# Kernel tuning notes

Measured on AMD Instinct MI355X. Metric: run time of the kernel, lower is better.

The kernel has to match this reference:

```python
import jax, jax.numpy as jnp
import numpy as np

H_IMG, W_IMG = 48, 64  # feature-map resolution hard-coded in the module
NUM_HEADS = 8


def get_positional_encodings(B, N, dtype=jnp.float32):
    # (p3^2, p4^2, p3*p4, p3, p4, 1) on normalized grid; intrinsics=None path
    ys = jnp.linspace(-1.0, 1.0, H_IMG, dtype=dtype)
    xs = jnp.linspace(-1.0, 1.0, W_IMG, dtype=dtype)
    p3 = jnp.tile(ys, W_IMG)           # [N] = ys repeated W times (torch repeat)
    p4 = jnp.repeat(xs, H_IMG)         # [N] = each x repeated H times
    pos = jnp.stack([p3 * p3, p4 * p4, p3 * p4, p3, p4, jnp.ones_like(p3)], axis=-1)  # [N,6]
    return jnp.broadcast_to(pos[None], (B, N, 6))


def setup_inputs() -> dict:
    key = jax.random.key(0)
    k1, k2, k3, k4, k5 = jax.random.split(key, 5)
    B, N, C = 2, H_IMG * W_IMG, 256
    s = 0.02
    return {
        "x1": jax.random.normal(k1, (B, N, C), jnp.float32),
        "x2": jax.random.normal(k2, (B, N, C), jnp.float32),
        "Wq": jax.random.normal(k3, (C, C), jnp.float32) * s,      # qkv (one-way: q only)
        "Wkv": jax.random.normal(k4, (C, 2 * C), jnp.float32) * s,  # qkv2 -> k,v
        "Wpf": jax.random.normal(k5, (C + 6 * NUM_HEADS, C), jnp.float32) * s,  # proj_fundamental
        "bpf": jnp.zeros((C,), jnp.float32),
    }


def reference(x1, x2, Wq, Wkv, Wpf, bpf):
    B, N, C = x1.shape
    H = NUM_HEADS
    d = C // H
    scale = d ** -0.5

    # q from x1; k,v from x2 (separate linear, matching torch reshape/permute split)
    q1 = (x1 @ Wq).reshape(B, N, H, d).transpose(0, 2, 1, 3)          # [B,H,N,d]
    kv = (x2 @ Wkv).reshape(B, N, 2, H, d)
    k2 = kv[:, :, 0].transpose(0, 2, 1, 3)                            # [B,H,N,d]
    v2 = kv[:, :, 1].transpose(0, 2, 1, 3)                            # [B,H,N,d]

    attn = jax.nn.softmax(jnp.einsum('bhnd,bhmd->bhnm', q1, k2) * scale, axis=-1)  # [B,H,N,N]

    pos = get_positional_encodings(B, N, x1.dtype)                    # [B,N,6]
    v2p = jnp.concatenate(
        [v2, jnp.broadcast_to(pos[:, None], (B, H, N, 6))], axis=-1)  # [B,H,N,d+6]

    y = jnp.einsum('bhnm,bhmd->bhnd', attn, v2p)                      # [B,H,N,d+6]
    y = y.transpose(0, 2, 1, 3).reshape(B, N, H * (d + 6))            # [B,N,C+6H]
    y = y @ Wpf + bpf                                                 # [B,N,C]
    y = y.reshape(B, N, H, d).transpose(0, 2, 1, 3)                   # [B,H,N,d]

    return jnp.concatenate([attn, y], axis=-1)                        # [B,H,N,N+d]
```

## Files before the change

kernel.cpp:

```cpp
#include <hip/hip_runtime.h>
#include <hip/hip_bf16.h>
#include <cstdint>
#include <cstddef>

#define NB 2
#define NH 8
#define BHN 16
#define NN 3072
#define CC 256
#define DD 32
#define OUTW 3104
#define VW 48
#define KP 384

typedef __attribute__((ext_vector_type(8))) __bf16 bf16x8;
typedef __attribute__((ext_vector_type(4))) short short4v;
typedef __attribute__((ext_vector_type(4))) float f32x4;

static __device__ __forceinline__ unsigned short f2bf(float f) {
    __hip_bfloat16 h = __float2bfloat16(f);
    return *reinterpret_cast<unsigned short*>(&h);
}

static __device__ __forceinline__ bf16x8 ldb8(const unsigned short* p) {
    return *(const bf16x8*)p;
}

static __device__ __forceinline__ f32x4 mfma16(bf16x8 a, bf16x8 b, f32x4 c) {
    return __builtin_amdgcn_mfma_f32_16x16x32_bf16(a, b, c, 0, 0, 0);
}

__global__ __launch_bounds__(256) void prep_kernel(
    const float* __restrict__ x1, const float* __restrict__ x2,
    const float* __restrict__ Wq, const float* __restrict__ Wkv,
    const float* __restrict__ Wpf,
    unsigned short* __restrict__ x1b, unsigned short* __restrict__ x2b,
    unsigned short* __restrict__ Wt, unsigned short* __restrict__ Wpft,
    unsigned short* __restrict__ v2pT)
{
    int i = blockIdx.x * 256 + threadIdx.x;
    const int S_X = NB * NN * CC;
    if (i < S_X) { x1b[i] = f2bf(x1[i]); return; }
    i -= S_X;
    if (i < S_X) { x2b[i] = f2bf(x2[i]); return; }
    i -= S_X;
    const int S_WT = 768 * CC;
    if (i < S_WT) {
        int j = i >> 8, kk = i & 255;
        float w = (j < 256) ? Wq[kk * 256 + j] : Wkv[kk * 512 + (j - 256)];
        Wt[i] = f2bf(w);
        return;
    }
    i -= S_WT;
    const int S_WP = 256 * KP;
    if (i < S_WP) {
        int c2 = i / KP, t = i - c2 * KP;
        int h = t / VW, cc = t - h * VW;
        unsigned short v = 0;
        if (cc < 38) v = f2bf(Wpf[(h * 38 + cc) * 256 + c2]);
        Wpft[i] = v;
        return;
    }
    i -= S_WP;
    const int S_POS = BHN * 16 * NN;
    if (i < S_POS) {
        int n = i % NN;
        int r = i / NN;
        int bh = r >> 4;
        int c = (r & 15) + 32;
        float val = 0.f;
        if (c < 38) {
            float p3 = -1.f + 2.f * (float)(n % 48) / 47.f;
            float p4 = -1.f + 2.f * (float)(n / 48) / 63.f;
            float pv[6] = { p3 * p3, p4 * p4, p3 * p4, p3, p4, 1.f };
            val = pv[c - 32];
        }
        v2pT[((size_t)bh * VW + c) * NN + n] = f2bf(val);
    }
}

__global__ __launch_bounds__(256) void qkv_kernel(
    const unsigned short* __restrict__ x1b, const unsigned short* __restrict__ x2b,
    const unsigned short* __restrict__ Wt,
    unsigned short* __restrict__ qbh, unsigned short* __restrict__ kbh,
    unsigned short* __restrict__ v2pT)
{
    int rt = blockIdx.x, ct = blockIdx.y;
    int wv = threadIdx.x >> 6, lane = threadIdx.x & 63;
    int g = lane >> 4, q = lane & 15;
    int row0 = rt * 64 + wv * 16;
    const unsigned short* A = (ct < 4) ? x1b : x2b;
    const unsigned short* arow = A + (size_t)(row0 + q) * CC + g * 8;
    const unsigned short* brow = Wt + (size_t)(ct * 64 + q) * CC + g * 8;
    f32x4 acc[4];
    #pragma unroll
    for (int cb = 0; cb < 4; ++cb) acc[cb] = f32x4{0.f, 0.f, 0.f, 0.f};
    for (int k0 = 0; k0 < CC; k0 += 32) {
        bf16x8 af = ldb8(arow + k0);
        #pragma unroll
        for (int cb = 0; cb < 4; ++cb)
            acc[cb] = mfma16(af, ldb8(brow + (size_t)cb * 16 * CC + k0), acc[cb]);
    }
    int b = row0 / NN, nb = row0 % NN;
    #pragma unroll
    for (int cb = 0; cb < 4; ++cb) {
        int jj = ct * 64 + cb * 16 + q;
        #pragma unroll
        for (int r = 0; r < 4; ++r) {
            int n = nb + 4 * g + r;
            unsigned short bv = f2bf(acc[cb][r]);
            if (jj < 256) {
                int h = jj >> 5, c = jj & 31;
                qbh[(size_t)((b * NH + h) * NN + n) * DD + c] = bv;
            } else if (jj < 512) {
                int jk = jj - 256; int h = jk >> 5, c = jk & 31;
                kbh[(size_t)((b * NH + h) * NN + n) * DD + c] = bv;
            } else {
                int jv = jj - 512; int h = jv >> 5, c = jv & 31;
                v2pT[(size_t)((b * NH + h) * VW + c) * NN + n] = bv;
            }
        }
    }
}

__global__ __launch_bounds__(256, 4) void attn_kernel(
    const unsigned short* __restrict__ qbh, const unsigned short* __restrict__ kbh,
    const unsigned short* __restrict__ v2pT,
    float* __restrict__ out, unsigned short* __restrict__ yacc)
{
    __shared__ unsigned short plds[4][16][40];
    __shared__ float lsum[4][16];
    __shared__ float yl[4][48][17];
    const float C = 0.17677669529663687f * 1.4426950408889634f;

    int bh = blockIdx.x;
    int qt = blockIdx.y;
    int wv = threadIdx.x >> 6, lane = threadIdx.x & 63;
    int g = lane >> 4, q = lane & 15;
    int qrow = qt * 16;
    int mbase = wv * 768;

    bf16x8 qf = ldb8(qbh + (size_t)(bh * NN + qrow + q) * DD + g * 8);
    const unsigned short* kbase = kbh + (size_t)bh * NN * DD;
    const unsigned short* vbase = v2pT + (size_t)bh * VW * NN;

    float l = 0.f;
    {
        bf16x8 kf0 = ldb8(kbase + (size_t)(mbase + q) * DD + g * 8);
        bf16x8 kf1 = ldb8(kbase + (size_t)(mbase + 16 + q) * DD + g * 8);
        for (int it = 0; it < 24; ++it) {
            int m0 = mbase + it * 32;
            bf16x8 kn0 = ldb8(kbase + (size_t)(m0 + 32 + q) * DD + g * 8);
            bf16x8 kn1 = ldb8(kbase + (size_t)(m0 + 48 + q) * DD + g * 8);
            f32x4 z = {0.f, 0.f, 0.f, 0.f};
            f32x4 s0 = mfma16(kf0, qf, z);
            f32x4 s1 = mfma16(kf1, qf, z);
            #pragma unroll
            for (int r = 0; r < 4; ++r)
                l += exp2f(s0[r] * C) + exp2f(s1[r] * C);
            kf0 = kn0; kf1 = kn1;
        }
    }
    l += __shfl_xor(l, 16, 64);
    l += __shfl_xor(l, 32, 64);
    if (lane < 16) lsum[wv][q] = l;
    __syncthreads();
    float ltot = lsum[0][q] + lsum[1][q] + lsum[2][q] + lsum[3][q];
    float nl2 = -__log2f(ltot);

    f32x4 yt0 = {0.f,0.f,0.f,0.f}, yt1 = yt0, yt2 = yt0;
    float* orow = out + (size_t)(bh * NN + qrow + q) * OUTW;
    unsigned short* pl = &plds[wv][q][0];

    bf16x8 kf0 = ldb8(kbase + (size_t)(mbase + q) * DD + g * 8);
    bf16x8 kf1 = ldb8(kbase + (size_t)(mbase + 16 + q) * DD + g * 8);
    for (int it = 0; it < 24; ++it) {
        int m0 = mbase + it * 32;
        bf16x8 kn0 = ldb8(kbase + (size_t)(m0 + 32 + q) * DD + g * 8);
        bf16x8 kn1 = ldb8(kbase + (size_t)(m0 + 48 + q) * DD + g * 8);
        bf16x8 vf0 = ldb8(vbase + (size_t)(q) * NN + m0 + g * 8);
        bf16x8 vf1 = ldb8(vbase + (size_t)(16 + q) * NN + m0 + g * 8);
        bf16x8 vf2 = ldb8(vbase + (size_t)(32 + q) * NN + m0 + g * 8);

        f32x4 z = {0.f, 0.f, 0.f, 0.f};
        f32x4 s0 = mfma16(kf0, qf, z);
        f32x4 s1 = mfma16(kf1, qf, z);
        f32x4 p0, p1;
        #pragma unroll
        for (int r = 0; r < 4; ++r) {
            p0[r] = exp2f(__builtin_fmaf(s0[r], C, nl2));
            p1[r] = exp2f(__builtin_fmaf(s1[r], C, nl2));
        }
        __builtin_nontemporal_store(p0, (f32x4*)(orow + m0 + 4 * g));
        __builtin_nontemporal_store(p1, (f32x4*)(orow + m0 + 16 + 4 * g));

        short4v pk0, pk1;
        #pragma unroll
        for (int r = 0; r < 4; ++r) {
            pk0[r] = (short)f2bf(p0[r]);
            pk1[r] = (short)f2bf(p1[r]);
        }
        *(short4v*)(pl + 4 * g) = pk0;
        *(short4v*)(pl + 16 + 4 * g) = pk1;
        asm volatile("s_waitcnt lgkmcnt(0)" ::: "memory");
        __builtin_amdgcn_sched_barrier(0);
        bf16x8 pf = ldb8(pl + 8 * g);
        yt0 = mfma16(vf0, pf, yt0);
        yt1 = mfma16(vf1, pf, yt1);
        yt2 = mfma16(vf2, pf, yt2);
        kf0 = kn0; kf1 = kn1;
    }

    {
        f32x4 yts[3] = { yt0, yt1, yt2 };
        #pragma unroll
        for (int cb = 0; cb < 3; ++cb)
            #pragma unroll
            for (int r = 0; r < 4; ++r)
                yl[wv][cb * 16 + 4 * g + r][q] = yts[cb][r];
    }
    __syncthreads();
    if (wv < 3) {
        int cb = wv;
        int b = bh >> 3, h = bh & 7;
        unsigned short* yrow = yacc + (size_t)(b * NN + qrow + q) * KP + h * VW;
        short4v pk;
        #pragma unroll
        for (int r = 0; r < 4; ++r) {
            int c = cb * 16 + 4 * g + r;
            float s = yl[0][c][q] + yl[1][c][q] + yl[2][c][q] + yl[3][c][q];
            pk[r] = (short)f2bf(s);
        }
        *(short4v*)(yrow + cb * 16 + 4 * g) = pk;
    }
}

__global__ __launch_bounds__(256) void proj_kernel(
    const unsigned short* __restrict__ yacc, const unsigned short* __restrict__ Wpft,
    const float* __restrict__ bpf, float* __restrict__ out)
{
    int rt = blockIdx.x, ct = blockIdx.y;
    int wv = threadIdx.x >> 6, lane = threadIdx.x & 63;
    int g = lane >> 4, q = lane & 15;
    int row0 = rt * 64 + wv * 16;
    const unsigned short* arow = yacc + (size_t)(row0 + q) * KP + g * 8;
    const unsigned short* b0 = Wpft + (size_t)(ct * 64 + q) * KP + g * 8;
    f32x4 acc[4];
    #pragma unroll
    for (int cb = 0; cb < 4; ++cb) acc[cb] = f32x4{0.f, 0.f, 0.f, 0.f};
    for (int k0 = 0; k0 < KP; k0 += 32) {
        bf16x8 af = ldb8(arow + k0);
        #pragma unroll
        for (int cb = 0; cb < 4; ++cb)
            acc[cb] = mfma16(af, ldb8(b0 + (size_t)cb * 16 * KP + k0), acc[cb]);
    }
    int b = row0 / NN, nb = row0 % NN;
    #pragma unroll
    for (int cb = 0; cb < 4; ++cb) {
        int c2 = ct * 64 + cb * 16 + q;
        float bias = bpf[c2];
        int h = c2 >> 5, c = c2 & 31;
        float* obase = out + (size_t)((b * NH + h) * NN) * OUTW + NN + c;
        #pragma unroll
        for (int r = 0; r < 4; ++r) {
            int n = nb + 4 * g + r;
            __builtin_nontemporal_store(acc[cb][r] + bias, &obase[(size_t)n * OUTW]);
        }
    }
}

extern "C" void kernel_launch(void* const* d_in, const int* in_sizes, int n_in,
                              void* d_out, int out_size, void* d_ws, size_t ws_size,
                              hipStream_t stream)
{
    (void)in_sizes; (void)n_in; (void)out_size; (void)ws_size;
    const float* x1  = (const float*)d_in[0];
    const float* x2  = (const float*)d_in[1];
    const float* Wq  = (const float*)d_in[2];
    const float* Wkv = (const float*)d_in[3];
    const float* Wpf = (const float*)d_in[4];
    const float* bpf = (const float*)d_in[5];
    float* out = (float*)d_out;
    char* ws = (char*)d_ws;

    unsigned short* x1b  = (unsigned short*)(ws + 0);
    unsigned short* x2b  = (unsigned short*)(ws + 3145728);
    unsigned short* Wt   = (unsigned short*)(ws + 6291456);
    unsigned short* Wpft = (unsigned short*)(ws + 6684672);
    unsigned short* qbh  = (unsigned short*)(ws + 6881280);
    unsigned short* kbh  = (unsigned short*)(ws + 10027008);
    unsigned short* v2pT = (unsigned short*)(ws + 13172736);
    unsigned short* yacc = (unsigned short*)(ws + 17891328);

    prep_kernel<<<16512, 256, 0, stream>>>(x1, x2, Wq, Wkv, Wpf, x1b, x2b, Wt, Wpft, v2pT);
    qkv_kernel<<<dim3(96, 12), 256, 0, stream>>>(x1b, x2b, Wt, qbh, kbh, v2pT);
    attn_kernel<<<dim3(16, 192), 256, 0, stream>>>(qbh, kbh, v2pT, out, yacc);
    proj_kernel<<<dim3(96, 4), 256, 0, stream>>>(yacc, Wpft, bpf, out);
}
```

Baseline: 253.3 us.

## Process four query tiles per attention block and remap blocks by XCD

Each attention block now handles 64 query rows (four 16-row tiles) instead of 16, so every K and V fragment loaded from global memory is reused across four query tiles. The grid becomes a flat 768 blocks, with block IDs mapped so that each XCD works on two fixed (batch, head) pairs, which is meant to improve L2 locality for K/V. The P staging buffer now reuses the yl shared array, and the final reduction loops over all threads. Register pressure rises (launch bounds drop to 2 blocks per CU) and there are 4x fewer blocks, which may hurt occupancy and latency hiding.

New measurement: 274.5 us. +8.3%, slower.

```diff
diff --git a/kernel.cpp b/kernel.cpp
--- a/kernel.cpp
+++ b/kernel.cpp
@@ -123,28 +123,35 @@
     }
 }
 
-__global__ __launch_bounds__(256, 4) void attn_kernel(
+__global__ __launch_bounds__(256, 2) void attn_kernel(
     const unsigned short* __restrict__ qbh, const unsigned short* __restrict__ kbh,
     const unsigned short* __restrict__ v2pT,
     float* __restrict__ out, unsigned short* __restrict__ yacc)
 {
-    __shared__ unsigned short plds[4][16][40];
-    __shared__ float lsum[4][16];
-    __shared__ float yl[4][48][17];
+    __shared__ float yl[4][48][65];
+    __shared__ float lsum[4][64];
     const float C = 0.17677669529663687f * 1.4426950408889634f;
 
-    int bh = blockIdx.x;
-    int qt = blockIdx.y;
+    int id = blockIdx.x;
+    int xcd = id & 7;
+    int slot = id >> 3;
+    int bh = xcd * 2 + (slot & 1);
+    int qt = slot >> 1;
+
     int wv = threadIdx.x >> 6, lane = threadIdx.x & 63;
     int g = lane >> 4, q = lane & 15;
-    int qrow = qt * 16;
+    int qrow = qt * 64;
     int mbase = wv * 768;
 
-    bf16x8 qf = ldb8(qbh + (size_t)(bh * NN + qrow + q) * DD + g * 8);
     const unsigned short* kbase = kbh + (size_t)bh * NN * DD;
     const unsigned short* vbase = v2pT + (size_t)bh * VW * NN;
 
-    float l = 0.f;
+    bf16x8 qf[4];
+    #pragma unroll
+    for (int rt = 0; rt < 4; ++rt)
+        qf[rt] = ldb8(qbh + (size_t)(bh * NN + qrow + rt * 16 + q) * DD + g * 8);
+
+    float l[4] = {0.f, 0.f, 0.f, 0.f};
     {
         bf16x8 kf0 = ldb8(kbase + (size_t)(mbase + q) * DD + g * 8);
         bf16x8 kf1 = ldb8(kbase + (size_t)(mbase + 16 + q) * DD + g * 8);
@@ -152,25 +159,40 @@
             int m0 = mbase + it * 32;
             bf16x8 kn0 = ldb8(kbase + (size_t)(m0 + 32 + q) * DD + g * 8);
             bf16x8 kn1 = ldb8(kbase + (size_t)(m0 + 48 + q) * DD + g * 8);
-            f32x4 z = {0.f, 0.f, 0.f, 0.f};
-            f32x4 s0 = mfma16(kf0, qf, z);
-            f32x4 s1 = mfma16(kf1, qf, z);
-            #pragma unroll
-            for (int r = 0; r < 4; ++r)
-                l += exp2f(s0[r] * C) + exp2f(s1[r] * C);
+            #pragma unroll
+            for (int rt = 0; rt < 4; ++rt) {
+                f32x4 z = {0.f, 0.f, 0.f, 0.f};
+                f32x4 s0 = mfma16(kf0, qf[rt], z);
+                f32x4 s1 = mfma16(kf1, qf[rt], z);
+                #pragma unroll
+                for (int r = 0; r < 4; ++r)
+                    l[rt] += exp2f(s0[r] * C) + exp2f(s1[r] * C);
+            }
             kf0 = kn0; kf1 = kn1;
         }
     }
-    l += __shfl_xor(l, 16, 64);
-    l += __shfl_xor(l, 32, 64);
-    if (lane < 16) lsum[wv][q] = l;
+    #pragma unroll
+    for (int rt = 0; rt < 4; ++rt) {
+        l[rt] += __shfl_xor(l[rt], 16, 64);
+        l[rt] += __shfl_xor(l[rt], 32, 64);
+        if (lane < 16) lsum[wv][rt * 16 + q] = l[rt];
+    }
     __syncthreads();
-    float ltot = lsum[0][q] + lsum[1][q] + lsum[2][q] + lsum[3][q];
-    float nl2 = -__log2f(ltot);
-
-    f32x4 yt0 = {0.f,0.f,0.f,0.f}, yt1 = yt0, yt2 = yt0;
-    float* orow = out + (size_t)(bh * NN + qrow + q) * OUTW;
-    unsigned short* pl = &plds[wv][q][0];
+    float nl2[4];
+    #pragma unroll
+    for (int rt = 0; rt < 4; ++rt) {
+        int rr = rt * 16 + q;
+        nl2[rt] = -__log2f(lsum[0][rr] + lsum[1][rr] + lsum[2][rr] + lsum[3][rr]);
+    }
+
+    f32x4 yt[4][3];
+    #pragma unroll
+    for (int rt = 0; rt < 4; ++rt)
+        #pragma unroll
+        for (int cb = 0; cb < 3; ++cb)
+            yt[rt][cb] = f32x4{0.f, 0.f, 0.f, 0.f};
+
+    unsigned short* plbase = (unsigned short*)&yl[wv][0][0];
 
     bf16x8 kf0 = ldb8(kbase + (size_t)(mbase + q) * DD + g * 8);
     bf16x8 kf1 = ldb8(kbase + (size_t)(mbase + 16 + q) * DD + g * 8);
@@ -182,56 +204,63 @@
         bf16x8 vf1 = ldb8(vbase + (size_t)(16 + q) * NN + m0 + g * 8);
         bf16x8 vf2 = ldb8(vbase + (size_t)(32 + q) * NN + m0 + g * 8);
 
-        f32x4 z = {0.f, 0.f, 0.f, 0.f};
-        f32x4 s0 = mfma16(kf0, qf, z);
-        f32x4 s1 = mfma16(kf1, qf, z);
-        f32x4 p0, p1;
-        #pragma unroll
-        for (int r = 0; r < 4; ++r) {
-            p0[r] = exp2f(__builtin_fmaf(s0[r], C, nl2));
-            p1[r] = exp2f(__builtin_fmaf(s1[r], C, nl2));
-        }
-        __builtin_nontemporal_store(p0, (f32x4*)(orow + m0 + 4 * g));
-        __builtin_nontemporal_store(p1, (f32x4*)(orow + m0 + 16 + 4 * g));
-
-        short4v pk0, pk1;
-        #pragma unroll
-        for (int r = 0; r < 4; ++r) {
-            pk0[r] = (short)f2bf(p0[r]);
-            pk1[r] = (short)f2bf(p1[r]);
-        }
-        *(short4v*)(pl + 4 * g) = pk0;
-        *(short4v*)(pl + 16 + 4 * g) = pk1;
-        asm volatile("s_waitcnt lgkmcnt(0)" ::: "memory");
-        __builtin_amdgcn_sched_barrier(0);
-        bf16x8 pf = ldb8(pl + 8 * g);
-        yt0 = mfma16(vf0, pf, yt0);
-        yt1 = mfma16(vf1, pf, yt1);
-        yt2 = mfma16(vf2, pf, yt2);
+        #pragma unroll
+        for (int rt = 0; rt < 4; ++rt) {
+            f32x4 z = {0.f, 0.f, 0.f, 0.f};
+            f32x4 s0 = mfma16(kf0, qf[rt], z);
+            f32x4 s1 = mfma16(kf1, qf[rt], z);
+            f32x4 p0, p1;
+            #pragma unroll
+            for (int r = 0; r < 4; ++r) {
+                p0[r] = exp2f(__builtin_fmaf(s0[r], C, nl2[rt]));
+                p1[r] = exp2f(__builtin_fmaf(s1[r], C, nl2[rt]));
+            }
+            float* orow = out + (size_t)(bh * NN + qrow + rt * 16 + q) * OUTW;
+            __builtin_nontemporal_store(p0, (f32x4*)(orow + m0 + 4 * g));
+            __builtin_nontemporal_store(p1, (f32x4*)(orow + m0 + 16 + 4 * g));
+
+            short4v pk0, pk1;
+            #pragma unroll
+            for (int r = 0; r < 4; ++r) {
+                pk0[r] = (short)f2bf(p0[r]);
+                pk1[r] = (short)f2bf(p1[r]);
+            }
+            unsigned short* pl = plbase + q * 40;
+            *(short4v*)(pl + 4 * g) = pk0;
+            *(short4v*)(pl + 16 + 4 * g) = pk1;
+            asm volatile("s_waitcnt lgkmcnt(0)" ::: "memory");
+            __builtin_amdgcn_sched_barrier(0);
+            bf16x8 pf = ldb8(pl + 8 * g);
+            yt[rt][0] = mfma16(vf0, pf, yt[rt][0]);
+            yt[rt][1] = mfma16(vf1, pf, yt[rt][1]);
+            yt[rt][2] = mfma16(vf2, pf, yt[rt][2]);
+        }
         kf0 = kn0; kf1 = kn1;
     }
 
+    __syncthreads();
+    #pragma unroll
+    for (int rt = 0; rt < 4; ++rt)
+        #pragma unroll
+        for (int cb = 0; cb < 3; ++cb)
+            #pragma unroll
+            for (int r = 0; r < 4; ++r)
+                yl[wv][cb * 16 + 4 * g + r][rt * 16 + q] = yt[rt][cb][r];
+    __syncthreads();
     {
-        f32x4 yts[3] = { yt0, yt1, yt2 };
-        #pragma unroll
-        for (int cb = 0; cb < 3; ++cb)
-            #pragma unroll
-            for (int r = 0; r < 4; ++r)
-                yl[wv][cb * 16 + 4 * g + r][q] = yts[cb][r];
-    }
-    __syncthreads();
-    if (wv < 3) {
-        int cb = wv;
         int b = bh >> 3, h = bh & 7;
-        unsigned short* yrow = yacc + (size_t)(b * NN + qrow + q) * KP + h * VW;
-        short4v pk;
-        #pragma unroll
-        for (int r = 0; r < 4; ++r) {
-            int c = cb * 16 + 4 * g + r;
-            float s = yl[0][c][q] + yl[1][c][q] + yl[2][c][q] + yl[3][c][q];
-            pk[r] = (short)f2bf(s);
-        }
-        *(short4v*)(yrow + cb * 16 + 4 * g) = pk;
+        for (int t = threadIdx.x; t < 768; t += 256) {
+            int cg = t >> 6, n = t & 63;
+            short4v pk;
+            #pragma unroll
+            for (int j = 0; j < 4; ++j) {
+                int c = cg * 4 + j;
+                float s = yl[0][c][n] + yl[1][c][n] + yl[2][c][n] + yl[3][c][n];
+                pk[j] = (short)f2bf(s);
+            }
+            unsigned short* yrow = yacc + (size_t)(b * NN + qrow + n) * KP + h * VW;
+            *(short4v*)(yrow + cg * 4) = pk;
+        }
     }
 }
 
@@ -294,6 +323,6 @@
 
     prep_kernel<<<16512, 256, 0, stream>>>(x1, x2, Wq, Wkv, Wpf, x1b, x2b, Wt, Wpft, v2pT);
     qkv_kernel<<<dim3(96, 12), 256, 0, stream>>>(x1b, x2b, Wt, qbh, kbh, v2pT);
-    attn_kernel<<<dim3(16, 192), 256, 0, stream>>>(qbh, kbh, v2pT, out, yacc);
+    attn_kernel<<<768, 256, 0, stream>>>(qbh, kbh, v2pT, out, yacc);
     proj_kernel<<<dim3(96, 4), 256, 0, stream>>>(yacc, Wpft, bpf, out);
 }
```
